# Kernel optimization log

Hardware: AMD Instinct MI355X
Metric: run time of the kernel (lower is better)

Reference implementation:

```python
import jax, jax.numpy as jnp
import numpy as np

B, N, DIN, D, E, STEP = 4, 1024, 256, 256, 5, 5


def setup_inputs() -> dict:
    key = jax.random.key(0)
    ks = jax.random.split(key, 14)
    s = 0.02  # weight init scale
    inp = {
        "node_features": jax.random.normal(ks[0], (B, N, DIN), dtype=jnp.float32),
        # dense per-edge-type adjacency; scaled so messages stay in a sane range
        "adj_matrices": jax.random.uniform(ks[1], (B, E, N, N), dtype=jnp.float32) * (2.0 / N),
        "fc_in_w": jax.random.normal(ks[2], (D, DIN), dtype=jnp.float32) * s,
        "fc_in_b": jnp.zeros((D,), dtype=jnp.float32),
        "edge_w": jax.random.normal(ks[3], (E, D, D), dtype=jnp.float32) * s,
        "edge_b": jax.random.normal(ks[4], (E, D), dtype=jnp.float32) * s,
        "gru_w_ih": jax.random.normal(ks[5], (3 * D, D), dtype=jnp.float32) * s,
        "gru_w_hh": jax.random.normal(ks[6], (3 * D, D), dtype=jnp.float32) * s,
        "gru_b_ih": jnp.zeros((3 * D,), dtype=jnp.float32),
        "gru_b_hh": jnp.zeros((3 * D,), dtype=jnp.float32),
        "conv1_w": jax.random.normal(ks[7], (D, D), dtype=jnp.float32) * s,
        "conv1_b": jnp.zeros((D,), dtype=jnp.float32),
        "conv2_w": jax.random.normal(ks[8], (D, D), dtype=jnp.float32) * s,
        "conv2_b": jnp.zeros((D,), dtype=jnp.float32),
    }
    return inp


def _gru_cell(x, h, w_ih, w_hh, b_ih, b_hh):
    # torch GRUCell: gates ordered [r, z, n]
    gi = x @ w_ih.T + b_ih  # [B*N, 3D]
    gh = h @ w_hh.T + b_hh
    ir, iz, inn = jnp.split(gi, 3, axis=-1)
    hr, hz, hn = jnp.split(gh, 3, axis=-1)
    r = jax.nn.sigmoid(ir + hr)
    z = jax.nn.sigmoid(iz + hz)
    n = jnp.tanh(inn + r * hn)
    return (1.0 - z) * n + z * h


def reference(node_features, adj_matrices, fc_in_w, fc_in_b, edge_w, edge_b,
              gru_w_ih, gru_w_hh, gru_b_ih, gru_b_hh,
              conv1_w, conv1_b, conv2_w, conv2_b):
    h = node_features @ fc_in_w.T + fc_in_b  # [B, N, D]
    sum_edge_b = jnp.sum(edge_b, axis=0)  # accumulated biases over edge types
    for _ in range(STEP):
        # messages per edge type: adj_e @ h  -> [B, E, N, D]
        msgs = jnp.einsum('benm,bmd->bend', adj_matrices, h)
        # per-edge-type linear (y = x @ W_e.T) then accumulate over edge types
        acc = jnp.einsum('bend,ekd->bnk', msgs, edge_w) + sum_edge_b  # [B, N, D]
        h = _gru_cell(acc, h, gru_w_ih, gru_w_hh, gru_b_ih, gru_b_hh)
    node_states = h  # [B, N, D]
    # conv1d with kernel_size=1 over node axis == per-node linear on channels
    attn_weights = jax.nn.sigmoid(node_states @ conv1_w.T + conv1_b)  # [B, N, D]
    feats = jnp.tanh(node_states @ conv2_w.T + conv2_b)  # [B, N, D]
    graph_embedding = jnp.sum(attn_weights * feats, axis=1)  # sum over nodes -> [B, D]
    attn_map = jnp.mean(attn_weights, axis=2)  # mean over channels -> [B, N]
    return (graph_embedding, node_states, attn_map)
```

## Files before the change

kernel.cpp:

```cpp
#include <hip/hip_runtime.h>
#include <hip/hip_bf16.h>
#include <cstdint>


typedef __attribute__((ext_vector_type(8))) short bf16x8;
typedef __attribute__((ext_vector_type(4))) float f32x4;

__device__ __forceinline__ float bf2f(__hip_bfloat16 x) { return __bfloat162float(x); }
__device__ __forceinline__ __hip_bfloat16 f2bf(float x) { return __float2bfloat16(x); }
__device__ __forceinline__ short f2bs(float x) {
  __hip_bfloat16 h = __float2bfloat16(x);
  return *reinterpret_cast<short*>(&h);
}
__device__ __forceinline__ float s2f(short x) {
  __hip_bfloat16 h = *reinterpret_cast<__hip_bfloat16*>(&x);
  return __bfloat162float(h);
}

__device__ __forceinline__ bf16x8 ld8_ext(const void* base, long off, bool f32) {
  if (f32) {
    const float* p = (const float*)base + off;
    bf16x8 r;
#pragma unroll
    for (int i = 0; i < 8; ++i) r[i] = f2bs(p[i]);
    return r;
  }
  return *(const bf16x8*)((const __hip_bfloat16*)base + off);
}

__device__ __forceinline__ bf16x8 ld8_sum5(const __hip_bfloat16* part, int row, int k) {
  const long base = (long)row * 256 + (long)(row >> 10) * 1048576 + k;
  float s[8] = {0.f, 0.f, 0.f, 0.f, 0.f, 0.f, 0.f, 0.f};
#pragma unroll
  for (int e = 0; e < 5; ++e) {
    bf16x8 v = *(const bf16x8*)(part + base + e * 262144);
#pragma unroll
    for (int j = 0; j < 8; ++j) s[j] += s2f(v[j]);
  }
  bf16x8 r;
#pragma unroll
  for (int j = 0; j < 8; ++j) r[j] = f2bs(s[j]);
  return r;
}

__global__ void detect_dtype(const uint32_t* __restrict__ raw, int* __restrict__ flag) {
  __shared__ int cnt;
  if (threadIdx.x == 0) cnt = 0;
  __syncthreads();
  int c = 0;
  for (int i = threadIdx.x; i < 512; i += 256) {
    uint32_t byte = (raw[i] >> 8) & 0xFF;
    if (byte >= 0x28 && byte <= 0x40) ++c;
  }
  atomicAdd(&cnt, c);
  __syncthreads();
  if (threadIdx.x == 0) *flag = (cnt < 300) ? 1 : 0;
}

__global__ void prep_pool(const void* fcb, const void* bih, const void* bhh,
                          const void* c1b, const void* c2b, const void* edgeb,
                          const int* __restrict__ flag,
                          float* __restrict__ pool, float* __restrict__ ge,
                          float* __restrict__ am32) {
  const bool f32 = (*flag != 0);
  for (int t = threadIdx.x; t < 2560; t += 256) {
    const void* p; int i;
    if (t < 256)       { p = fcb;  i = t; }
    else if (t < 1024) { p = bih;  i = t - 256; }
    else if (t < 1792) { p = bhh;  i = t - 1024; }
    else if (t < 2048) { p = c1b;  i = t - 1792; }
    else if (t < 2304) { p = c2b;  i = t - 2048; }
    else {
      int k = t - 2304; float s = 0.f;
      for (int e = 0; e < 5; ++e)
        s += f32 ? ((const float*)edgeb)[e * 256 + k]
                 : bf2f(((const __hip_bfloat16*)edgeb)[e * 256 + k]);
      pool[t] = s; continue;
    }
    pool[t] = f32 ? ((const float*)p)[i] : bf2f(((const __hip_bfloat16*)p)[i]);
  }
  for (int t = threadIdx.x; t < 1024; t += 256) ge[t] = 0.f;
  for (int t = threadIdx.x; t < 4096; t += 256) am32[t] = 0.f;
}

__global__ void bias_gi_k(const float* __restrict__ pool,
                          const __hip_bfloat16* __restrict__ wih,
                          float* __restrict__ out) {
  const int n = blockIdx.x * 256 + threadIdx.x;
  if (n >= 768) return;
  float s = pool[256 + n];
  for (int k = 0; k < 256; ++k) s += pool[2304 + k] * bf2f(wih[n * 256 + k]);
  out[n] = s;
}

__global__ void wcvt_all(const void* fcw, const void* edw, const void* wih,
                         const void* whh, const void* c1w, const void* c2w,
                         const int* __restrict__ flag, __hip_bfloat16* __restrict__ dst) {
  const bool f32 = (*flag != 0);
  const int i = blockIdx.x * 256 + threadIdx.x;
  const void* src; int off;
  if      (i < 65536)  { src = fcw; off = i; }
  else if (i < 393216) { src = edw; off = i - 65536; }
  else if (i < 589824) { src = wih; off = i - 393216; }
  else if (i < 786432) { src = whh; off = i - 589824; }
  else if (i < 851968) { src = c1w; off = i - 786432; }
  else                 { src = c2w; off = i - 851968; }
  dst[i] = f32 ? f2bf(((const float*)src)[off])
               : ((const __hip_bfloat16*)src)[off];
}

__global__ void adj_cvt(const void* __restrict__ src, const int* __restrict__ flag,
                        __hip_bfloat16* __restrict__ dst) {
  const bool f32 = (*flag != 0);
  const long i = ((long)blockIdx.x * 256 + threadIdx.x) * 8;
  bf16x8 r;
  if (f32) {
    const float* p = (const float*)src + i;
#pragma unroll
    for (int j = 0; j < 8; ++j) r[j] = f2bs(p[j]);
  } else {
    r = *(const bf16x8*)((const __hip_bfloat16*)src + i);
  }
  *(bf16x8*)(dst + i) = r;
}

template<bool HAS_BIAS, bool DUAL>
__global__ __launch_bounds__(256)
void gemm_bt128(const __hip_bfloat16* __restrict__ A, const __hip_bfloat16* __restrict__ Bt,
                const float* __restrict__ bias, __hip_bfloat16* __restrict__ C,
                const __hip_bfloat16* __restrict__ A2, const __hip_bfloat16* __restrict__ Bt2,
                const float* __restrict__ bias2, __hip_bfloat16* __restrict__ C2,
                int K, int lda, int ldb, int ldc,
                long aBatch, int zdivA, int zmodA,
                long bBatch, int zdivB, int zmodB,
                long cBatch, int zdivC, int zSplit)
{
  __shared__ __align__(16) __hip_bfloat16 sA[128 * 64];
  __shared__ __align__(16) __hip_bfloat16 sB[64 * 64];
  const int t = threadIdx.x;
  const int w = t >> 6;
  const int l = t & 63;
  const int m0 = blockIdx.x * 128;
  const int n0 = blockIdx.y * 64;
  int z = blockIdx.z;

  const __hip_bfloat16* Au = A; const __hip_bfloat16* Btu = Bt;
  const float* biasu = bias; __hip_bfloat16* Cu = C;
  if (DUAL && z >= zSplit) { Au = A2; Btu = Bt2; biasu = bias2; Cu = C2; z -= zSplit; }

  const __hip_bfloat16* Ab = Au + (long)((z / zdivA) % zmodA) * aBatch;
  const __hip_bfloat16* Bb = Btu + (long)((z / zdivB) % zmodB) * bBatch;

  int sra[4], sca[4];
#pragma unroll
  for (int i = 0; i < 4; ++i) {
    const int p = t + 256 * i;
    sra[i] = p >> 3;
    sca[i] = (p & 7) ^ (sra[i] & 7);
  }
  const int p0 = t, p1 = t + 256;
  const int sr0 = p0 >> 3, sc0 = (p0 & 7) ^ (sr0 & 7);
  const int sr1 = p1 >> 3, sc1 = (p1 & 7) ^ (sr1 & 7);

  f32x4 acc[2][4];
#pragma unroll
  for (int i = 0; i < 2; ++i)
#pragma unroll
    for (int j = 0; j < 4; ++j) acc[i][j] = (f32x4){0.f, 0.f, 0.f, 0.f};

  const int r15 = l & 15;
  const int quad = l >> 4;

  for (int k0 = 0; k0 < K; k0 += 64) {
    bf16x8 av[4];
#pragma unroll
    for (int i = 0; i < 4; ++i)
      av[i] = *(const bf16x8*)(Ab + (long)(m0 + sra[i]) * lda + (k0 + sca[i] * 8));
    bf16x8 b0 = *(const bf16x8*)(Bb + (long)(n0 + sr0) * ldb + (k0 + sc0 * 8));
    bf16x8 b1 = *(const bf16x8*)(Bb + (long)(n0 + sr1) * ldb + (k0 + sc1 * 8));
    __syncthreads();
#pragma unroll
    for (int i = 0; i < 4; ++i) *(bf16x8*)(sA + (t + 256 * i) * 8) = av[i];
    *(bf16x8*)(sB + p0 * 8) = b0;
    *(bf16x8*)(sB + p1 * 8) = b1;
    __syncthreads();
#pragma unroll
    for (int ks = 0; ks < 2; ++ks) {
      const int cg = ks * 4 + quad;
      bf16x8 aF[2], bF[4];
#pragma unroll
      for (int mi = 0; mi < 2; ++mi) {
        const int row = mi * 64 + w * 16 + r15;
        aF[mi] = *(const bf16x8*)(sA + row * 64 + ((cg ^ (row & 7)) * 8));
      }
#pragma unroll
      for (int ni = 0; ni < 4; ++ni) {
        const int nrow = ni * 16 + r15;
        bF[ni] = *(const bf16x8*)(sB + nrow * 64 + ((cg ^ (nrow & 7)) * 8));
      }
#pragma unroll
      for (int mi = 0; mi < 2; ++mi)
#pragma unroll
        for (int ni = 0; ni < 4; ++ni)
          acc[mi][ni] = __builtin_amdgcn_mfma_f32_16x16x32_bf16(
              aF[mi], bF[ni], acc[mi][ni], 0, 0, 0);
    }
  }

  const long cOff = (long)(z / zdivC) * cBatch;
#pragma unroll
  for (int mi = 0; mi < 2; ++mi) {
#pragma unroll
    for (int ni = 0; ni < 4; ++ni) {
      const int n = n0 + ni * 16 + r15;
      float bv = 0.f;
      if (HAS_BIAS) bv = biasu[n];
#pragma unroll
      for (int r = 0; r < 4; ++r) {
        const int m = m0 + mi * 64 + w * 16 + quad * 4 + r;
        Cu[cOff + (long)m * ldc + n] = f2bf(acc[mi][ni][r] + bv);
      }
    }
  }
}

__global__ __launch_bounds__(256)
void part_gh(const __hip_bfloat16* __restrict__ adjb,
             const __hip_bfloat16* __restrict__ heT,
             __hip_bfloat16* __restrict__ part,
             const __hip_bfloat16* __restrict__ hbf,
             const __hip_bfloat16* __restrict__ whh,
             const float* __restrict__ bhh,
             __hip_bfloat16* __restrict__ gh)
{
  __shared__ __align__(16) __hip_bfloat16 sA[128 * 64];
  __shared__ __align__(16) __hip_bfloat16 sB[64 * 64];
  const int t = threadIdx.x;
  const int w = t >> 6;
  const int l = t & 63;
  const int bid = blockIdx.x;

  const __hip_bfloat16* Ab; const __hip_bfloat16* Bb;
  __hip_bfloat16* Cu; const float* biasu = nullptr;
  int K, lda, ldb, ldc, m0, n0;
  bool has_bias;
  if (bid < 640) {
    const int z = bid >> 5, rem = bid & 31;
    m0 = (rem & 7) * 128; n0 = (rem >> 3) * 64;
    Ab = adjb + (long)z * 1048576; lda = 1024; K = 1024;
    Bb = heT + (long)z * 262144;  ldb = 1024;
    Cu = part + (long)z * 262144; ldc = 256;
    has_bias = false;
  } else {
    const int idx = bid - 640;
    m0 = (idx & 31) * 128; n0 = (idx >> 5) * 64;
    Ab = hbf; lda = 256; K = 256;
    Bb = whh; ldb = 256;
    Cu = gh;  ldc = 768;
    biasu = bhh; has_bias = true;
  }

  int sra[4], sca[4];
#pragma unroll
  for (int i = 0; i < 4; ++i) {
    const int p = t + 256 * i;
    sra[i] = p >> 3;
    sca[i] = (p & 7) ^ (sra[i] & 7);
  }
  const int p0 = t, p1 = t + 256;
  const int sr0 = p0 >> 3, sc0 = (p0 & 7) ^ (sr0 & 7);
  const int sr1 = p1 >> 3, sc1 = (p1 & 7) ^ (sr1 & 7);

  f32x4 acc[2][4];
#pragma unroll
  for (int i = 0; i < 2; ++i)
#pragma unroll
    for (int j = 0; j < 4; ++j) acc[i][j] = (f32x4){0.f, 0.f, 0.f, 0.f};

  const int r15 = l & 15;
  const int quad = l >> 4;

  for (int k0 = 0; k0 < K; k0 += 64) {
    bf16x8 av[4];
#pragma unroll
    for (int i = 0; i < 4; ++i)
      av[i] = *(const bf16x8*)(Ab + (long)(m0 + sra[i]) * lda + (k0 + sca[i] * 8));
    bf16x8 b0 = *(const bf16x8*)(Bb + (long)(n0 + sr0) * ldb + (k0 + sc0 * 8));
    bf16x8 b1 = *(const bf16x8*)(Bb + (long)(n0 + sr1) * ldb + (k0 + sc1 * 8));
    __syncthreads();
#pragma unroll
    for (int i = 0; i < 4; ++i) *(bf16x8*)(sA + (t + 256 * i) * 8) = av[i];
    *(bf16x8*)(sB + p0 * 8) = b0;
    *(bf16x8*)(sB + p1 * 8) = b1;
    __syncthreads();
#pragma unroll
    for (int ks = 0; ks < 2; ++ks) {
      const int cg = ks * 4 + quad;
      bf16x8 aF[2], bF[4];
#pragma unroll
      for (int mi = 0; mi < 2; ++mi) {
        const int row = mi * 64 + w * 16 + r15;
        aF[mi] = *(const bf16x8*)(sA + row * 64 + ((cg ^ (row & 7)) * 8));
      }
#pragma unroll
      for (int ni = 0; ni < 4; ++ni) {
        const int nrow = ni * 16 + r15;
        bF[ni] = *(const bf16x8*)(sB + nrow * 64 + ((cg ^ (nrow & 7)) * 8));
      }
#pragma unroll
      for (int mi = 0; mi < 2; ++mi)
#pragma unroll
        for (int ni = 0; ni < 4; ++ni)
          acc[mi][ni] = __builtin_amdgcn_mfma_f32_16x16x32_bf16(
              aF[mi], bF[ni], acc[mi][ni], 0, 0, 0);
    }
  }

#pragma unroll
  for (int mi = 0; mi < 2; ++mi) {
#pragma unroll
    for (int ni = 0; ni < 4; ++ni) {
      const int n = n0 + ni * 16 + r15;
      const float bv = has_bias ? biasu[n] : 0.f;
#pragma unroll
      for (int r = 0; r < 4; ++r) {
        const int m = m0 + mi * 64 + w * 16 + quad * 4 + r;
        Cu[(long)m * ldc + n] = f2bf(acc[mi][ni][r] + bv);
      }
    }
  }
}

__global__ __launch_bounds__(256)
void gi_gate(const __hip_bfloat16* __restrict__ part,
             const __hip_bfloat16* __restrict__ wih,
             const float* __restrict__ biasgi,
             const __hip_bfloat16* __restrict__ gh,
             __hip_bfloat16* __restrict__ hbf,
             void* __restrict__ ns_out, const int* __restrict__ flag)
{
  __shared__ __align__(16) __hip_bfloat16 sA[64 * 64];
  __shared__ __align__(16) __hip_bfloat16 sB0[64 * 64];
  __shared__ __align__(16) __hip_bfloat16 sB1[64 * 64];
  __shared__ __align__(16) __hip_bfloat16 sB2[64 * 64];
  const int t = threadIdx.x;
  const int w = t >> 6;
  const int l = t & 63;
  const int m0 = (blockIdx.x & 63) * 64;
  const int n0 = (blockIdx.x >> 6) * 64;

  const int p0 = t, p1 = t + 256;
  const int sr0 = p0 >> 3, sc0 = (p0 & 7) ^ (sr0 & 7);
  const int sr1 = p1 >> 3, sc1 = (p1 & 7) ^ (sr1 & 7);

  f32x4 acc[3][4];
#pragma unroll
  for (int g = 0; g < 3; ++g)
#pragma unroll
    for (int j = 0; j < 4; ++j) acc[g][j] = (f32x4){0.f, 0.f, 0.f, 0.f};

  const int mrow = w * 16 + (l & 15);
  const int r15 = l & 15;
  const int quad = l >> 4;

  for (int k0 = 0; k0 < 256; k0 += 64) {
    bf16x8 a0 = ld8_sum5(part, m0 + sr0, k0 + sc0 * 8);
    bf16x8 a1 = ld8_sum5(part, m0 + sr1, k0 + sc1 * 8);
    bf16x8 bg[3][2];
#pragma unroll
    for (int g = 0; g < 3; ++g) {
      bg[g][0] = *(const bf16x8*)(wih + (long)(g * 256 + n0 + sr0) * 256 + (k0 + sc0 * 8));
      bg[g][1] = *(const bf16x8*)(wih + (long)(g * 256 + n0 + sr1) * 256 + (k0 + sc1 * 8));
    }
    __syncthreads();
    *(bf16x8*)(sA + p0 * 8) = a0;
    *(bf16x8*)(sA + p1 * 8) = a1;
    *(bf16x8*)(sB0 + p0 * 8) = bg[0][0]; *(bf16x8*)(sB0 + p1 * 8) = bg[0][1];
    *(bf16x8*)(sB1 + p0 * 8) = bg[1][0]; *(bf16x8*)(sB1 + p1 * 8) = bg[1][1];
    *(bf16x8*)(sB2 + p0 * 8) = bg[2][0]; *(bf16x8*)(sB2 + p1 * 8) = bg[2][1];
    __syncthreads();
#pragma unroll
    for (int ks = 0; ks < 2; ++ks) {
      const int cg = ks * 4 + quad;
      bf16x8 af = *(const bf16x8*)(sA + mrow * 64 + ((cg ^ (mrow & 7)) * 8));
#pragma unroll
      for (int t4 = 0; t4 < 4; ++t4) {
        const int nrow = t4 * 16 + r15;
        const int so = nrow * 64 + ((cg ^ (nrow & 7)) * 8);
        bf16x8 b0f = *(const bf16x8*)(sB0 + so);
        bf16x8 b1f = *(const bf16x8*)(sB1 + so);
        bf16x8 b2f = *(const bf16x8*)(sB2 + so);
        acc[0][t4] = __builtin_amdgcn_mfma_f32_16x16x32_bf16(af, b0f, acc[0][t4], 0, 0, 0);
        acc[1][t4] = __builtin_amdgcn_mfma_f32_16x16x32_bf16(af, b1f, acc[1][t4], 0, 0, 0);
        acc[2][t4] = __builtin_amdgcn_mfma_f32_16x16x32_bf16(af, b2f, acc[2][t4], 0, 0, 0);
      }
    }
  }

  const bool f32out = ns_out && (*flag != 0);
#pragma unroll
  for (int t4 = 0; t4 < 4; ++t4) {
    const int n = n0 + t4 * 16 + r15;
    const float bgr = biasgi[n];
    const float bgz = biasgi[256 + n];
    const float bgn = biasgi[512 + n];
#pragma unroll
    for (int r = 0; r < 4; ++r) {
      const int m = m0 + w * 16 + quad * 4 + r;
      const long gb = (long)m * 768;
      const float ir = acc[0][t4][r] + bgr;
      const float iz = acc[1][t4][r] + bgz;
      const float inn = acc[2][t4][r] + bgn;
      const float hr = bf2f(gh[gb + n]);
      const float hz = bf2f(gh[gb + 256 + n]);
      const float hn = bf2f(gh[gb + 512 + n]);
      const long hidx = (long)m * 256 + n;
      const float h = bf2f(hbf[hidx]);
      const float rr = 1.f / (1.f + __expf(-(ir + hr)));
      const float zz = 1.f / (1.f + __expf(-(iz + hz)));
      const float nn = tanhf(inn + rr * hn);
      const float hnew = (1.f - zz) * nn + zz * h;
      const __hip_bfloat16 hb = f2bf(hnew);
      hbf[hidx] = hb;
      if (ns_out) {
        if (f32out) ((float*)ns_out)[1024 + hidx] = hnew;
        else        ((__hip_bfloat16*)ns_out)[1024 + hidx] = hb;
      }
    }
  }
}

template<int OUT_MODE, bool HAS_BIAS, int A_MODE, bool DUAL>
__global__ __launch_bounds__(256)
void gemm_bt(const void* __restrict__ A, const __hip_bfloat16* __restrict__ Bt,
             const float* __restrict__ bias, void* __restrict__ Cp,
             const void* __restrict__ A2, const __hip_bfloat16* __restrict__ Bt2,
             const float* __restrict__ bias2, void* __restrict__ Cp2,
             const int* __restrict__ flag,
             int Kg, int ngrp, int lda, int ldb, int ldc,
             long aBatch, int zdivA, int zmodA,
             long bBatch, int zdivB, int zmodB,
             long cBatch, int zdivC, long aGrp, long bGrp, int zSplit)
{
  __shared__ __align__(16) __hip_bfloat16 sA[64 * 64];
  __shared__ __align__(16) __hip_bfloat16 sB[64 * 64];
  const bool af32 = (A_MODE == 1) ? (*flag != 0) : false;
  const int t = threadIdx.x;
  const int w = t >> 6;
  const int l = t & 63;
  const int m0 = blockIdx.x * 64;
  const int n0 = blockIdx.y * 64;
  int z = blockIdx.z;

  const void* Au = A; const __hip_bfloat16* Btu = Bt;
  const float* biasu = bias; void* Cpu = Cp;
  bool second = false;
  if (DUAL && z >= zSplit) {
    Au = A2; Btu = Bt2; biasu = bias2; Cpu = Cp2; z -= zSplit; second = true;
  }

  const long aOff = (long)((z / zdivA) % zmodA) * aBatch;
  const __hip_bfloat16* Bb = Btu + (long)((z / zdivB) % zmodB) * bBatch;

  const int p0 = t, p1 = t + 256;
  const int sr0 = p0 >> 3, sc0 = (p0 & 7) ^ (sr0 & 7);
  const int sr1 = p1 >> 3, sc1 = (p1 & 7) ^ (sr1 & 7);

  f32x4 acc[4];
#pragma unroll
  for (int i = 0; i < 4; ++i) acc[i] = (f32x4){0.f, 0.f, 0.f, 0.f};

  const int mrow = w * 16 + (l & 15);
  const int quad = l >> 4;

  for (int g = 0; g < ngrp; ++g) {
    const long aG = aOff + (long)g * aGrp;
    const __hip_bfloat16* Bg = Bb + (long)g * bGrp;
    for (int k0 = 0; k0 < Kg; k0 += 64) {
      bf16x8 a0, a1;
      if (A_MODE == 2 && !second) {
        a0 = ld8_sum5((const __hip_bfloat16*)Au, m0 + sr0, k0 + sc0 * 8);
        a1 = ld8_sum5((const __hip_bfloat16*)Au, m0 + sr1, k0 + sc1 * 8);
      } else if (A_MODE == 1) {
        a0 = ld8_ext(Au, aG + (long)(m0 + sr0) * lda + (k0 + sc0 * 8), af32);
        a1 = ld8_ext(Au, aG + (long)(m0 + sr1) * lda + (k0 + sc1 * 8), af32);
      } else {
        const __hip_bfloat16* Ab = (const __hip_bfloat16*)Au;
        a0 = *(const bf16x8*)(Ab + aG + (long)(m0 + sr0) * lda + (k0 + sc0 * 8));
        a1 = *(const bf16x8*)(Ab + aG + (long)(m0 + sr1) * lda + (k0 + sc1 * 8));
      }
      bf16x8 b0 = *(const bf16x8*)(Bg + (long)(n0 + sr0) * ldb + (k0 + sc0 * 8));
      bf16x8 b1 = *(const bf16x8*)(Bg + (long)(n0 + sr1) * ldb + (k0 + sc1 * 8));
      __syncthreads();
      *(bf16x8*)(sA + p0 * 8) = a0;
      *(bf16x8*)(sA + p1 * 8) = a1;
      *(bf16x8*)(sB + p0 * 8) = b0;
      *(bf16x8*)(sB + p1 * 8) = b1;
      __syncthreads();
#pragma unroll
      for (int ks = 0; ks < 2; ++ks) {
        const int cg = ks * 4 + quad;
        bf16x8 af = *(const bf16x8*)(sA + mrow * 64 + ((cg ^ (mrow & 7)) * 8));
#pragma unroll
        for (int t4 = 0; t4 < 4; ++t4) {
          const int nrow = t4 * 16 + (l & 15);
          bf16x8 bfr = *(const bf16x8*)(sB + nrow * 64 + ((cg ^ (nrow & 7)) * 8));
          acc[t4] = __builtin_amdgcn_mfma_f32_16x16x32_bf16(af, bfr, acc[t4], 0, 0, 0);
        }
      }
    }
  }

  const long cOff = (long)(z / zdivC) * cBatch;
#pragma unroll
  for (int t4 = 0; t4 < 4; ++t4) {
    const int n = n0 + t4 * 16 + (l & 15);
    float bv = 0.f;
    if (HAS_BIAS) bv = biasu[n];
#pragma unroll
    for (int r = 0; r < 4; ++r) {
      const int m = m0 + w * 16 + quad * 4 + r;
      const float v = acc[t4][r] + bv;
      if (OUT_MODE == 0)
        ((__hip_bfloat16*)Cpu)[cOff + (long)m * ldc + n] = f2bf(v);
      else
        ((float*)Cpu)[cOff + (long)m * ldc + n] = v;
    }
  }
}

__global__ void gru_gate8(const __hip_bfloat16* __restrict__ gi,
                          const __hip_bfloat16* __restrict__ gh,
                          __hip_bfloat16* __restrict__ hbf,
                          void* __restrict__ ns_out, const int* __restrict__ flag)
{
  const int t = blockIdx.x * 256 + threadIdx.x;
  const int m = t >> 5;
  const int k = (t & 31) * 8;
  const long gb = (long)m * 768 + k;
  bf16x8 vir = *(const bf16x8*)(gi + gb);
  bf16x8 viz = *(const bf16x8*)(gi + gb + 256);
  bf16x8 vin = *(const bf16x8*)(gi + gb + 512);
  bf16x8 vhr = *(const bf16x8*)(gh + gb);
  bf16x8 vhz = *(const bf16x8*)(gh + gb + 256);
  bf16x8 vhn = *(const bf16x8*)(gh + gb + 512);
  const long hidx = (long)m * 256 + k;
  bf16x8 vh = *(const bf16x8*)(hbf + hidx);
  bf16x8 out;
  float hf[8];
#pragma unroll
  for (int j = 0; j < 8; ++j) {
    const float r = 1.f / (1.f + __expf(-(s2f(vir[j]) + s2f(vhr[j]))));
    const float zz = 1.f / (1.f + __expf(-(s2f(viz[j]) + s2f(vhz[j]))));
    const float nn = tanhf(s2f(vin[j]) + r * s2f(vhn[j]));
    hf[j] = (1.f - zz) * nn + zz * s2f(vh[j]);
    out[j] = f2bs(hf[j]);
  }
  *(bf16x8*)(hbf + hidx) = out;
  if (ns_out) {
    if (*flag) {
      float* o = (float*)ns_out + 1024 + hidx;
#pragma unroll
      for (int j = 0; j < 8; ++j) o[j] = hf[j];
    } else {
      *(bf16x8*)((__hip_bfloat16*)ns_out + 1024 + hidx) = out;
    }
  }
}

__global__ __launch_bounds__(256)
void conv_fused(const __hip_bfloat16* __restrict__ hbf,
                const __hip_bfloat16* __restrict__ c1w,
                const __hip_bfloat16* __restrict__ c2w,
                const float* __restrict__ pool,
                float* __restrict__ geg, float* __restrict__ am32)
{
  __shared__ __align__(16) __hip_bfloat16 sA[64 * 64];
  __shared__ __align__(16) __hip_bfloat16 sB1[64 * 64];
  __shared__ __align__(16) __hip_bfloat16 sB2[64 * 64];
  __shared__ float sge[64];
  __shared__ float sam[64];
  const int t = threadIdx.x, w = t >> 6, l = t & 63;
  const int m0 = blockIdx.x * 64, n0 = blockIdx.y * 64;
  if (t < 64) { sge[t] = 0.f; sam[t] = 0.f; }
  const int p0 = t, p1 = t + 256;
  const int sr0 = p0 >> 3, sc0 = (p0 & 7) ^ (sr0 & 7);
  const int sr1 = p1 >> 3, sc1 = (p1 & 7) ^ (sr1 & 7);
  f32x4 a1[4], a2[4];
#pragma unroll
  for (int i = 0; i < 4; ++i) { a1[i] = (f32x4){0,0,0,0}; a2[i] = (f32x4){0,0,0,0}; }
  const int mrow = w * 16 + (l & 15);
  const int quad = l >> 4;
  for (int k0 = 0; k0 < 256; k0 += 64) {
    bf16x8 va0 = *(const bf16x8*)(hbf + (long)(m0 + sr0) * 256 + (k0 + sc0 * 8));
    bf16x8 va1 = *(const bf16x8*)(hbf + (long)(m0 + sr1) * 256 + (k0 + sc1 * 8));
    bf16x8 vb0 = *(const bf16x8*)(c1w + (long)(n0 + sr0) * 256 + (k0 + sc0 * 8));
    bf16x8 vb1 = *(const bf16x8*)(c1w + (long)(n0 + sr1) * 256 + (k0 + sc1 * 8));
    bf16x8 vc0 = *(const bf16x8*)(c2w + (long)(n0 + sr0) * 256 + (k0 + sc0 * 8));
    bf16x8 vc1 = *(const bf16x8*)(c2w + (long)(n0 + sr1) * 256 + (k0 + sc1 * 8));
    __syncthreads();
    *(bf16x8*)(sA + p0 * 8) = va0;  *(bf16x8*)(sA + p1 * 8) = va1;
    *(bf16x8*)(sB1 + p0 * 8) = vb0; *(bf16x8*)(sB1 + p1 * 8) = vb1;
    *(bf16x8*)(sB2 + p0 * 8) = vc0; *(bf16x8*)(sB2 + p1 * 8) = vc1;
    __syncthreads();
#pragma unroll
    for (int ks = 0; ks < 2; ++ks) {
      const int cg = ks * 4 + quad;
      bf16x8 af = *(const bf16x8*)(sA + mrow * 64 + ((cg ^ (mrow & 7)) * 8));
#pragma unroll
      for (int t4 = 0; t4 < 4; ++t4) {
        const int nrow = t4 * 16 + (l & 15);
        bf16x8 b1f = *(const bf16x8*)(sB1 + nrow * 64 + ((cg ^ (nrow & 7)) * 8));
        bf16x8 b2f = *(const bf16x8*)(sB2 + nrow * 64 + ((cg ^ (nrow & 7)) * 8));
        a1[t4] = __builtin_amdgcn_mfma_f32_16x16x32_bf16(af, b1f, a1[t4], 0, 0, 0);
        a2[t4] = __builtin_amdgcn_mfma_f32_16x16x32_bf16(af, b2f, a2[t4], 0, 0, 0);
      }
    }
  }
  float asum[4] = {0.f, 0.f, 0.f, 0.f};
#pragma unroll
  for (int t4 = 0; t4 < 4; ++t4) {
    const int n = n0 + t4 * 16 + (l & 15);
    const float bb1 = pool[1792 + n], bb2 = pool[2048 + n];
    float g = 0.f;
#pragma unroll
    for (int r = 0; r < 4; ++r) {
      const float av = 1.f / (1.f + __expf(-(a1[t4][r] + bb1)));
      const float fv = tanhf(a2[t4][r] + bb2);
      g += av * fv;
      asum[r] += av;
    }
    atomicAdd(&sge[t4 * 16 + (l & 15)], g);
  }
#pragma unroll
  for (int r = 0; r < 4; ++r) atomicAdd(&sam[w * 16 + quad * 4 + r], asum[r]);
  __syncthreads();
  if (t < 64) atomicAdd(&geg[(m0 >> 10) * 256 + n0 + t], sge[t]);
  else if (t < 128) atomicAdd(&am32[m0 + (t - 64)], sam[t - 64]);
}

__global__ void finish_out(const float* __restrict__ ge, const float* __restrict__ am32,
                           void* __restrict__ dout, const int* __restrict__ flag)
{
  const int t = blockIdx.x * 256 + threadIdx.x;
  const bool f32 = (*flag != 0);
  if (t < 1024) {
    if (f32) ((float*)dout)[t] = ge[t];
    else     ((__hip_bfloat16*)dout)[t] = f2bf(ge[t]);
  } else {
    const float v = am32[t - 1024] * (1.f / 256.f);
    if (f32) ((float*)dout)[1049600 + t - 1024] = v;
    else     ((__hip_bfloat16*)dout)[1049600 + t - 1024] = f2bf(v);
  }
}

extern "C" void kernel_launch(void* const* d_in, const int* in_sizes, int n_in,
                              void* d_out, int out_size, void* d_ws, size_t ws_size,
                              hipStream_t stream) {
  (void)in_sizes; (void)n_in; (void)out_size;
  const void* node_f = d_in[0];
  const void* adj    = d_in[1];
  const void* fc_w   = d_in[2];
  const void* fc_b   = d_in[3];
  const void* edge_w = d_in[4];
  const void* edge_b = d_in[5];
  const void* w_ih   = d_in[6];
  const void* w_hh   = d_in[7];
  const void* b_ih   = d_in[8];
  const void* b_hh   = d_in[9];
  const void* c1w    = d_in[10];
  const void* c1b    = d_in[11];
  const void* c2w    = d_in[12];
  const void* c2b    = d_in[13];

  char* ws = (char*)d_ws;
  const size_t MB = (size_t)1 << 20;
  int*            flag = (int*)(ws);
  float*          bp   = (float*)(ws + 256);
  float*          ge   = (float*)(ws + 14336);
  float*          am32 = (float*)(ws + 18432);
  __hip_bfloat16* wbf  = (__hip_bfloat16*)(ws + 34816);
  __hip_bfloat16* hbf  = (__hip_bfloat16*)(ws + 1869824);
  char*           S    = ws + 3966976;
  __hip_bfloat16* heT  = (__hip_bfloat16*)(S);
  __hip_bfloat16* part = (__hip_bfloat16*)(S + 10 * MB);
  __hip_bfloat16* gi   = (__hip_bfloat16*)(S + 20 * MB);
  __hip_bfloat16* gh   = (__hip_bfloat16*)(S + 26 * MB);
  __hip_bfloat16* adjb = (__hip_bfloat16*)(ws + 40 * MB);

  const bool has_split = ws_size >= 38 * MB;
  const bool has_adjb  = ws_size >= 81 * MB;

  detect_dtype<<<1, 256, 0, stream>>>((const uint32_t*)adj, flag);
  prep_pool<<<1, 256, 0, stream>>>(fc_b, b_ih, b_hh, c1b, c2b, edge_b, flag, bp, ge, am32);
  wcvt_all<<<3584, 256, 0, stream>>>(fc_w, edge_w, w_ih, w_hh, c1w, c2w, flag, wbf);
  bias_gi_k<<<3, 256, 0, stream>>>(bp, wbf + 393216, bp + 2560);
  if (has_adjb) adj_cvt<<<10240, 256, 0, stream>>>(adj, flag, adjb);

  gemm_bt<0, true, 1, false><<<dim3(64, 4, 1), 256, 0, stream>>>(
      node_f, wbf + 0, bp + 0, hbf, nullptr, nullptr, nullptr, nullptr, flag,
      256, 1, 256, 256, 256, 0, 1, 1, 0, 1, 1, 0, 1, 0, 0, 0);

  for (int s = 0; s < 5; ++s) {
    if (has_adjb) {
      gemm_bt128<false, false><<<dim3(2, 16, 20), 256, 0, stream>>>(
          wbf + 65536, hbf, nullptr, heT, nullptr, nullptr, nullptr, nullptr,
          256, 256, 256, 1024,
          65536, 1, 5,
          262144, 5, 4,
          262144, 1, 0);
      part_gh<<<1024, 256, 0, stream>>>(adjb, heT, part,
                                        hbf, wbf + 589824, bp + 1024, gh);
      gi_gate<<<256, 256, 0, stream>>>(part, wbf + 393216, bp + 2560, gh, hbf,
                                       (s == 4) ? d_out : nullptr, flag);
    } else if (has_split) {
      gemm_bt<0, false, 0, false><<<dim3(4, 16, 20), 256, 0, stream>>>(
          wbf + 65536, hbf, nullptr, heT, nullptr, nullptr, nullptr, nullptr, flag,
          256, 1, 256, 256, 1024,
          65536, 1, 5, 262144, 5, 4,
          262144, 1, 0, 0, 0);
      gemm_bt<0, false, 1, false><<<dim3(16, 4, 20), 256, 0, stream>>>(
          adj, heT, nullptr, part, nullptr, nullptr, nullptr, nullptr, flag,
          1024, 1, 1024, 1024, 256,
          1048576, 1, 20, 262144, 1, 20,
          262144, 1, 0, 0, 0);
      gemm_bt<0, true, 2, true><<<dim3(64, 12, 2), 256, 0, stream>>>(
          part, wbf + 393216, bp + 2560, gi,
          hbf,  wbf + 589824, bp + 1024, gh, flag,
          256, 1, 256, 256, 768, 0, 1, 1, 0, 1, 1, 0, 1, 0, 0, 1);
      gru_gate8<<<512, 256, 0, stream>>>(gi, gh, hbf,
                                         (s == 4) ? d_out : nullptr, flag);
    } else {
      gemm_bt<0, false, 0, false><<<dim3(4, 16, 20), 256, 0, stream>>>(
          wbf + 65536, hbf, nullptr, heT, nullptr, nullptr, nullptr, nullptr, flag,
          256, 1, 256, 256, 1024,
          65536, 1, 5, 262144, 5, 4,
          262144, 1, 0, 0, 0);
      gemm_bt<0, true, 1, false><<<dim3(16, 4, 4), 256, 0, stream>>>(
          adj, heT, bp + 2304, part, nullptr, nullptr, nullptr, nullptr, flag,
          1024, 5, 1024, 1024, 256,
          (long)5 * 1048576, 1, 4, (long)5 * 262144, 1, 4,
          262144, 1, 1048576, 262144, 0);
      gemm_bt<0, true, 0, true><<<dim3(64, 12, 2), 256, 0, stream>>>(
          part, wbf + 393216, bp + 256, gi,
          hbf,  wbf + 589824, bp + 1024, gh, flag,
          256, 1, 256, 256, 768, 0, 1, 1, 0, 1, 1, 0, 1, 0, 0, 1);
      gru_gate8<<<512, 256, 0, stream>>>(gi, gh, hbf,
                                         (s == 4) ? d_out : nullptr, flag);
    }
  }

  conv_fused<<<dim3(64, 4), 256, 0, stream>>>(hbf, wbf + 786432, wbf + 851968,
                                              bp, ge, am32);
  finish_out<<<20, 256, 0, stream>>>(ge, am32, d_out, flag);
}
```

Baseline: 432.8 us.

## Load B operand fragments directly from global memory instead of staging in LDS

The tiled GEMMs (heT, part/gh, gi_gate, and the readout kernel) no longer stage the B operand through shared memory. Each lane reads its MFMA B fragment straight from global memory through precomputed row pointers, and the duplicated tile loops are folded into one shared device helper. This cuts LDS traffic and shared-memory footprint, which may allow more blocks per CU, in exchange for uncoalesced, redundant global/L2 reads of B across the waves in a block. The heT launch is also moved to a flat 1D grid using the shared helper.

```diff
diff --git a/kernel.cpp b/kernel.cpp
--- a/kernel.cpp
+++ b/kernel.cpp
@@ -124,33 +124,13 @@
   *(bf16x8*)(dst + i) = r;
 }
 
-template<bool HAS_BIAS, bool DUAL>
-__global__ __launch_bounds__(256)
-void gemm_bt128(const __hip_bfloat16* __restrict__ A, const __hip_bfloat16* __restrict__ Bt,
-                const float* __restrict__ bias, __hip_bfloat16* __restrict__ C,
-                const __hip_bfloat16* __restrict__ A2, const __hip_bfloat16* __restrict__ Bt2,
-                const float* __restrict__ bias2, __hip_bfloat16* __restrict__ C2,
-                int K, int lda, int ldb, int ldc,
-                long aBatch, int zdivA, int zmodA,
-                long bBatch, int zdivB, int zmodB,
-                long cBatch, int zdivC, int zSplit)
-{
-  __shared__ __align__(16) __hip_bfloat16 sA[128 * 64];
-  __shared__ __align__(16) __hip_bfloat16 sB[64 * 64];
-  const int t = threadIdx.x;
-  const int w = t >> 6;
-  const int l = t & 63;
-  const int m0 = blockIdx.x * 128;
-  const int n0 = blockIdx.y * 64;
-  int z = blockIdx.z;
-
-  const __hip_bfloat16* Au = A; const __hip_bfloat16* Btu = Bt;
-  const float* biasu = bias; __hip_bfloat16* Cu = C;
-  if (DUAL && z >= zSplit) { Au = A2; Btu = Bt2; biasu = bias2; Cu = C2; z -= zSplit; }
-
-  const __hip_bfloat16* Ab = Au + (long)((z / zdivA) % zmodA) * aBatch;
-  const __hip_bfloat16* Bb = Btu + (long)((z / zdivB) % zmodB) * bBatch;
-
+__device__ __forceinline__ void tile128bd(__hip_bfloat16* sA, int t,
+    const __hip_bfloat16* Ab, int lda,
+    const __hip_bfloat16* Bb, int ldb,
+    const float* bias, __hip_bfloat16* C, int ldc,
+    int K, int m0, int n0)
+{
+  const int w = t >> 6, l = t & 63;
   int sra[4], sca[4];
 #pragma unroll
   for (int i = 0; i < 4; ++i) {
@@ -158,9 +138,6 @@
     sra[i] = p >> 3;
     sca[i] = (p & 7) ^ (sra[i] & 7);
   }
-  const int p0 = t, p1 = t + 256;
-  const int sr0 = p0 >> 3, sc0 = (p0 & 7) ^ (sr0 & 7);
-  const int sr1 = p1 >> 3, sc1 = (p1 & 7) ^ (sr1 & 7);
 
   f32x4 acc[2][4];
 #pragma unroll
@@ -171,34 +148,33 @@
   const int r15 = l & 15;
   const int quad = l >> 4;
 
+  const __hip_bfloat16* Brow[4];
+#pragma unroll
+  for (int ni = 0; ni < 4; ++ni)
+    Brow[ni] = Bb + (long)(n0 + ni * 16 + r15) * ldb;
+
   for (int k0 = 0; k0 < K; k0 += 64) {
     bf16x8 av[4];
 #pragma unroll
     for (int i = 0; i < 4; ++i)
       av[i] = *(const bf16x8*)(Ab + (long)(m0 + sra[i]) * lda + (k0 + sca[i] * 8));
-    bf16x8 b0 = *(const bf16x8*)(Bb + (long)(n0 + sr0) * ldb + (k0 + sc0 * 8));
-    bf16x8 b1 = *(const bf16x8*)(Bb + (long)(n0 + sr1) * ldb + (k0 + sc1 * 8));
     __syncthreads();
 #pragma unroll
     for (int i = 0; i < 4; ++i) *(bf16x8*)(sA + (t + 256 * i) * 8) = av[i];
-    *(bf16x8*)(sB + p0 * 8) = b0;
-    *(bf16x8*)(sB + p1 * 8) = b1;
     __syncthreads();
 #pragma unroll
     for (int ks = 0; ks < 2; ++ks) {
       const int cg = ks * 4 + quad;
       bf16x8 aF[2], bF[4];
+#pragma unroll
+      for (int ni = 0; ni < 4; ++ni)
+        bF[ni] = *(const bf16x8*)(Brow[ni] + k0 + cg * 8);
 #pragma unroll
       for (int mi = 0; mi < 2; ++mi) {
         const int row = mi * 64 + w * 16 + r15;
         aF[mi] = *(const bf16x8*)(sA + row * 64 + ((cg ^ (row & 7)) * 8));
       }
 #pragma unroll
-      for (int ni = 0; ni < 4; ++ni) {
-        const int nrow = ni * 16 + r15;
-        bF[ni] = *(const bf16x8*)(sB + nrow * 64 + ((cg ^ (nrow & 7)) * 8));
-      }
-#pragma unroll
       for (int mi = 0; mi < 2; ++mi)
 #pragma unroll
         for (int ni = 0; ni < 4; ++ni)
@@ -207,21 +183,35 @@
     }
   }
 
-  const long cOff = (long)(z / zdivC) * cBatch;
+  const bool hasb = (bias != nullptr);
 #pragma unroll
   for (int mi = 0; mi < 2; ++mi) {
 #pragma unroll
     for (int ni = 0; ni < 4; ++ni) {
       const int n = n0 + ni * 16 + r15;
-      float bv = 0.f;
-      if (HAS_BIAS) bv = biasu[n];
+      const float bv = hasb ? bias[n] : 0.f;
 #pragma unroll
       for (int r = 0; r < 4; ++r) {
         const int m = m0 + mi * 64 + w * 16 + quad * 4 + r;
-        Cu[cOff + (long)m * ldc + n] = f2bf(acc[mi][ni][r] + bv);
+        C[(long)m * ldc + n] = f2bf(acc[mi][ni][r] + bv);
       }
     }
   }
+}
+
+__global__ __launch_bounds__(256)
+void heT_k(const __hip_bfloat16* __restrict__ wbf,
+           const __hip_bfloat16* __restrict__ hbf,
+           __hip_bfloat16* __restrict__ heT)
+{
+  __shared__ __align__(16) __hip_bfloat16 sA[128 * 64];
+  const int bid = blockIdx.x;
+  const int z = bid >> 5, rem = bid & 31;
+  const int m0 = (rem & 1) * 128, n0 = (rem >> 1) * 64;
+  tile128bd(sA, threadIdx.x,
+            wbf + 65536 + (z % 5) * 65536, 256,
+            hbf + (long)(z / 5) * 262144, 256,
+            nullptr, heT + (long)z * 262144, 1024, 256, m0, n0);
 }
 
 __global__ __launch_bounds__(256)
@@ -234,100 +224,18 @@
              __hip_bfloat16* __restrict__ gh)
 {
   __shared__ __align__(16) __hip_bfloat16 sA[128 * 64];
-  __shared__ __align__(16) __hip_bfloat16 sB[64 * 64];
-  const int t = threadIdx.x;
-  const int w = t >> 6;
-  const int l = t & 63;
   const int bid = blockIdx.x;
-
-  const __hip_bfloat16* Ab; const __hip_bfloat16* Bb;
-  __hip_bfloat16* Cu; const float* biasu = nullptr;
-  int K, lda, ldb, ldc, m0, n0;
-  bool has_bias;
   if (bid < 640) {
     const int z = bid >> 5, rem = bid & 31;
-    m0 = (rem & 7) * 128; n0 = (rem >> 3) * 64;
-    Ab = adjb + (long)z * 1048576; lda = 1024; K = 1024;
-    Bb = heT + (long)z * 262144;  ldb = 1024;
-    Cu = part + (long)z * 262144; ldc = 256;
-    has_bias = false;
+    tile128bd(sA, threadIdx.x,
+              adjb + (long)z * 1048576, 1024,
+              heT + (long)z * 262144, 1024,
+              nullptr, part + (long)z * 262144, 256, 1024,
+              (rem & 7) * 128, (rem >> 3) * 64);
   } else {
     const int idx = bid - 640;
-    m0 = (idx & 31) * 128; n0 = (idx >> 5) * 64;
-    Ab = hbf; lda = 256; K = 256;
-    Bb = whh; ldb = 256;
-    Cu = gh;  ldc = 768;
-    biasu = bhh; has_bias = true;
-  }
-
-  int sra[4], sca[4];
-#pragma unroll
-  for (int i = 0; i < 4; ++i) {
-    const int p = t + 256 * i;
-    sra[i] = p >> 3;
-    sca[i] = (p & 7) ^ (sra[i] & 7);
-  }
-  const int p0 = t, p1 = t + 256;
-  const int sr0 = p0 >> 3, sc0 = (p0 & 7) ^ (sr0 & 7);
-  const int sr1 = p1 >> 3, sc1 = (p1 & 7) ^ (sr1 & 7);
-
-  f32x4 acc[2][4];
-#pragma unroll
-  for (int i = 0; i < 2; ++i)
-#pragma unroll
-    for (int j = 0; j < 4; ++j) acc[i][j] = (f32x4){0.f, 0.f, 0.f, 0.f};
-
-  const int r15 = l & 15;
-  const int quad = l >> 4;
-
-  for (int k0 = 0; k0 < K; k0 += 64) {
-    bf16x8 av[4];
-#pragma unroll
-    for (int i = 0; i < 4; ++i)
-      av[i] = *(const bf16x8*)(Ab + (long)(m0 + sra[i]) * lda + (k0 + sca[i] * 8));
-    bf16x8 b0 = *(const bf16x8*)(Bb + (long)(n0 + sr0) * ldb + (k0 + sc0 * 8));
-    bf16x8 b1 = *(const bf16x8*)(Bb + (long)(n0 + sr1) * ldb + (k0 + sc1 * 8));
-    __syncthreads();
-#pragma unroll
-    for (int i = 0; i < 4; ++i) *(bf16x8*)(sA + (t + 256 * i) * 8) = av[i];
-    *(bf16x8*)(sB + p0 * 8) = b0;
-    *(bf16x8*)(sB + p1 * 8) = b1;
-    __syncthreads();
-#pragma unroll
-    for (int ks = 0; ks < 2; ++ks) {
-      const int cg = ks * 4 + quad;
-      bf16x8 aF[2], bF[4];
-#pragma unroll
-      for (int mi = 0; mi < 2; ++mi) {
-        const int row = mi * 64 + w * 16 + r15;
-        aF[mi] = *(const bf16x8*)(sA + row * 64 + ((cg ^ (row & 7)) * 8));
-      }
-#pragma unroll
-      for (int ni = 0; ni < 4; ++ni) {
-        const int nrow = ni * 16 + r15;
-        bF[ni] = *(const bf16x8*)(sB + nrow * 64 + ((cg ^ (nrow & 7)) * 8));
-      }
-#pragma unroll
-      for (int mi = 0; mi < 2; ++mi)
-#pragma unroll
-        for (int ni = 0; ni < 4; ++ni)
-          acc[mi][ni] = __builtin_amdgcn_mfma_f32_16x16x32_bf16(
-              aF[mi], bF[ni], acc[mi][ni], 0, 0, 0);
-    }
-  }
-
-#pragma unroll
-  for (int mi = 0; mi < 2; ++mi) {
-#pragma unroll
-    for (int ni = 0; ni < 4; ++ni) {
-      const int n = n0 + ni * 16 + r15;
-      const float bv = has_bias ? biasu[n] : 0.f;
-#pragma unroll
-      for (int r = 0; r < 4; ++r) {
-        const int m = m0 + mi * 64 + w * 16 + quad * 4 + r;
-        Cu[(long)m * ldc + n] = f2bf(acc[mi][ni][r] + bv);
-      }
-    }
+    tile128bd(sA, threadIdx.x, hbf, 256, whh, 256, bhh, gh, 768, 256,
+              (idx & 31) * 128, (idx >> 5) * 64);
   }
 }
 
@@ -340,9 +248,6 @@
              void* __restrict__ ns_out, const int* __restrict__ flag)
 {
   __shared__ __align__(16) __hip_bfloat16 sA[64 * 64];
-  __shared__ __align__(16) __hip_bfloat16 sB0[64 * 64];
-  __shared__ __align__(16) __hip_bfloat16 sB1[64 * 64];
-  __shared__ __align__(16) __hip_bfloat16 sB2[64 * 64];
   const int t = threadIdx.x;
   const int w = t >> 6;
   const int l = t & 63;
@@ -363,21 +268,19 @@
   const int r15 = l & 15;
   const int quad = l >> 4;
 
+  const __hip_bfloat16* Brow[3][4];
+#pragma unroll
+  for (int g = 0; g < 3; ++g)
+#pragma unroll
+    for (int ni = 0; ni < 4; ++ni)
+      Brow[g][ni] = wih + (long)(g * 256 + n0 + ni * 16 + r15) * 256;
+
   for (int k0 = 0; k0 < 256; k0 += 64) {
     bf16x8 a0 = ld8_sum5(part, m0 + sr0, k0 + sc0 * 8);
     bf16x8 a1 = ld8_sum5(part, m0 + sr1, k0 + sc1 * 8);
-    bf16x8 bg[3][2];
-#pragma unroll
-    for (int g = 0; g < 3; ++g) {
-      bg[g][0] = *(const bf16x8*)(wih + (long)(g * 256 + n0 + sr0) * 256 + (k0 + sc0 * 8));
-      bg[g][1] = *(const bf16x8*)(wih + (long)(g * 256 + n0 + sr1) * 256 + (k0 + sc1 * 8));
-    }
     __syncthreads();
     *(bf16x8*)(sA + p0 * 8) = a0;
     *(bf16x8*)(sA + p1 * 8) = a1;
-    *(bf16x8*)(sB0 + p0 * 8) = bg[0][0]; *(bf16x8*)(sB0 + p1 * 8) = bg[0][1];
-    *(bf16x8*)(sB1 + p0 * 8) = bg[1][0]; *(bf16x8*)(sB1 + p1 * 8) = bg[1][1];
-    *(bf16x8*)(sB2 + p0 * 8) = bg[2][0]; *(bf16x8*)(sB2 + p1 * 8) = bg[2][1];
     __syncthreads();
 #pragma unroll
     for (int ks = 0; ks < 2; ++ks) {
@@ -385,11 +288,9 @@
       bf16x8 af = *(const bf16x8*)(sA + mrow * 64 + ((cg ^ (mrow & 7)) * 8));
 #pragma unroll
       for (int t4 = 0; t4 < 4; ++t4) {
-        const int nrow = t4 * 16 + r15;
-        const int so = nrow * 64 + ((cg ^ (nrow & 7)) * 8);
-        bf16x8 b0f = *(const bf16x8*)(sB0 + so);
-        bf16x8 b1f = *(const bf16x8*)(sB1 + so);
-        bf16x8 b2f = *(const bf16x8*)(sB2 + so);
+        bf16x8 b0f = *(const bf16x8*)(Brow[0][t4] + k0 + cg * 8);
+        bf16x8 b1f = *(const bf16x8*)(Brow[1][t4] + k0 + cg * 8);
+        bf16x8 b2f = *(const bf16x8*)(Brow[2][t4] + k0 + cg * 8);
         acc[0][t4] = __builtin_amdgcn_mfma_f32_16x16x32_bf16(af, b0f, acc[0][t4], 0, 0, 0);
         acc[1][t4] = __builtin_amdgcn_mfma_f32_16x16x32_bf16(af, b1f, acc[1][t4], 0, 0, 0);
         acc[2][t4] = __builtin_amdgcn_mfma_f32_16x16x32_bf16(af, b2f, acc[2][t4], 0, 0, 0);
@@ -576,8 +477,6 @@
                 float* __restrict__ geg, float* __restrict__ am32)
 {
   __shared__ __align__(16) __hip_bfloat16 sA[64 * 64];
-  __shared__ __align__(16) __hip_bfloat16 sB1[64 * 64];
-  __shared__ __align__(16) __hip_bfloat16 sB2[64 * 64];
   __shared__ float sge[64];
   __shared__ float sam[64];
   const int t = threadIdx.x, w = t >> 6, l = t & 63;
@@ -590,18 +489,21 @@
 #pragma unroll
   for (int i = 0; i < 4; ++i) { a1[i] = (f32x4){0,0,0,0}; a2[i] = (f32x4){0,0,0,0}; }
   const int mrow = w * 16 + (l & 15);
+  const int r15 = l & 15;
   const int quad = l >> 4;
+  const __hip_bfloat16* B1row[4];
+  const __hip_bfloat16* B2row[4];
+#pragma unroll
+  for (int ni = 0; ni < 4; ++ni) {
+    B1row[ni] = c1w + (long)(n0 + ni * 16 + r15) * 256;
+    B2row[ni] = c2w + (long)(n0 + ni * 16 + r15) * 256;
+  }
   for (int k0 = 0; k0 < 256; k0 += 64) {
     bf16x8 va0 = *(const bf16x8*)(hbf + (long)(m0 + sr0) * 256 + (k0 + sc0 * 8));
     bf16x8 va1 = *(const bf16x8*)(hbf + (long)(m0 + sr1) * 256 + (k0 + sc1 * 8));
-    bf16x8 vb0 = *(const bf16x8*)(c1w + (long)(n0 + sr0) * 256 + (k0 + sc0 * 8));
-    bf16x8 vb1 = *(const bf16x8*)(c1w + (long)(n0 + sr1) * 256 + (k0 + sc1 * 8));
-    bf16x8 vc0 = *(const bf16x8*)(c2w + (long)(n0 + sr0) * 256 + (k0 + sc0 * 8));
-    bf16x8 vc1 = *(const bf16x8*)(c2w + (long)(n0 + sr1) * 256 + (k0 + sc1 * 8));
     __syncthreads();
-    *(bf16x8*)(sA + p0 * 8) = va0;  *(bf16x8*)(sA + p1 * 8) = va1;
-    *(bf16x8*)(sB1 + p0 * 8) = vb0; *(bf16x8*)(sB1 + p1 * 8) = vb1;
-    *(bf16x8*)(sB2 + p0 * 8) = vc0; *(bf16x8*)(sB2 + p1 * 8) = vc1;
+    *(bf16x8*)(sA + p0 * 8) = va0;
+    *(bf16x8*)(sA + p1 * 8) = va1;
     __syncthreads();
 #pragma unroll
     for (int ks = 0; ks < 2; ++ks) {
@@ -609,9 +511,8 @@
       bf16x8 af = *(const bf16x8*)(sA + mrow * 64 + ((cg ^ (mrow & 7)) * 8));
 #pragma unroll
       for (int t4 = 0; t4 < 4; ++t4) {
-        const int nrow = t4 * 16 + (l & 15);
-        bf16x8 b1f = *(const bf16x8*)(sB1 + nrow * 64 + ((cg ^ (nrow & 7)) * 8));
-        bf16x8 b2f = *(const bf16x8*)(sB2 + nrow * 64 + ((cg ^ (nrow & 7)) * 8));
+        bf16x8 b1f = *(const bf16x8*)(B1row[t4] + k0 + cg * 8);
+        bf16x8 b2f = *(const bf16x8*)(B2row[t4] + k0 + cg * 8);
         a1[t4] = __builtin_amdgcn_mfma_f32_16x16x32_bf16(af, b1f, a1[t4], 0, 0, 0);
         a2[t4] = __builtin_amdgcn_mfma_f32_16x16x32_bf16(af, b2f, a2[t4], 0, 0, 0);
       }
@@ -703,12 +604,7 @@
 
   for (int s = 0; s < 5; ++s) {
     if (has_adjb) {
-      gemm_bt128<false, false><<<dim3(2, 16, 20), 256, 0, stream>>>(
-          wbf + 65536, hbf, nullptr, heT, nullptr, nullptr, nullptr, nullptr,
-          256, 256, 256, 1024,
-          65536, 1, 5,
-          262144, 5, 4,
-          262144, 1, 0);
+      heT_k<<<640, 256, 0, stream>>>(wbf, hbf, heT);
       part_gh<<<1024, 256, 0, stream>>>(adjb, heT, part,
                                         hbf, wbf + 589824, bp + 1024, gh);
       gi_gate<<<256, 256, 0, stream>>>(part, wbf + 393216, bp + 2560, gh, hbf,
```

New measurement: 662.5 us. 1.53x slower.
